# Kernel optimization log

Measured on AMD Instinct MI355X. Metric: run time of the kernel, lower is better.

## Reference

```python
import jax, jax.numpy as jnp
from jax import lax
import numpy as np

K = 4          # kernel_size
DEPTH = 2      # sig_depth
B, S, CIN = 64, 1024, 5
H1, H2 = 64, 16
OUT = 32
C1 = H2 + CIN + 1            # channels entering signature1 (include_original + include_time)
SIG_C1 = C1 + C1 * C1        # 506
SIG_C2 = H2 + H2 * H2        # 272


def setup_inputs() -> dict:
    key = jax.random.key(0)
    ks = jax.random.split(key, 12)
    def w(k, shape, fan_in):
        return jax.random.normal(k, shape, jnp.float32) * (1.0 / np.sqrt(fan_in))
    inp = {}
    inp["x"] = jax.random.normal(ks[0], (B, S, CIN), jnp.float32)
    inp["lengths"] = jax.random.randint(ks[1], (B,), S // 2, S + 1)
    # Augment 1: Conv1d(CIN->H1, k=K), Conv1d(H1->H1, 1), Conv1d(H1->H2, 1)
    inp["a1_w0"] = w(ks[2], (H1, CIN, K), CIN * K); inp["a1_b0"] = jnp.zeros((H1,), jnp.float32)
    inp["a1_w1"] = w(ks[3], (H1, H1, 1), H1);       inp["a1_b1"] = jnp.zeros((H1,), jnp.float32)
    inp["a1_w2"] = w(ks[4], (H2, H1, 1), H1);       inp["a1_b2"] = jnp.zeros((H2,), jnp.float32)
    # Augment 2: Conv1d(SIG_C1->H1, k=K), Conv1d(H1->H1, 1), Conv1d(H1->H2, 1)
    inp["a2_w0"] = w(ks[5], (H1, SIG_C1, K), SIG_C1 * K); inp["a2_b0"] = jnp.zeros((H1,), jnp.float32)
    inp["a2_w1"] = w(ks[6], (H1, H1, 1), H1);             inp["a2_b1"] = jnp.zeros((H1,), jnp.float32)
    inp["a2_w2"] = w(ks[7], (H2, H1, 1), H1);             inp["a2_b2"] = jnp.zeros((H2,), jnp.float32)
    inp["lin_w"] = w(ks[8], (OUT, SIG_C2), SIG_C2)
    inp["lin_b"] = jnp.zeros((OUT,), jnp.float32)
    return inp


def _conv1d(x, w, b):
    # x: (B, C, L), w: (O, I, k) -> (B, O, L-k+1), VALID (no padding), stride 1
    y = lax.conv_general_dilated(x, w, (1,), 'VALID', dimension_numbers=('NCH', 'OIH', 'NCH'))
    return y + b[None, :, None]


def _augment(x, ws, bs, kernel_size, include_original, include_time):
    # signatory.Augment: relu between convs, none after last; concat [original_trunc, time, conv_out]
    b_, s_, _ = x.shape
    L = s_ - kernel_size + 1
    pieces = []
    if include_original:
        pieces.append(x[:, kernel_size - 1:, :])
    if include_time:
        t = jnp.linspace(0.0, 1.0, L, dtype=x.dtype)
        pieces.append(jnp.broadcast_to(t[None, :, None], (b_, L, 1)))
    h = jnp.swapaxes(x, 1, 2)
    h = _conv1d(h, ws[0], bs[0])
    for wi, bi in zip(ws[1:], bs[1:]):
        h = _conv1d(jax.nn.relu(h), wi, bi)
    pieces.append(jnp.swapaxes(h, 1, 2))
    return jnp.concatenate(pieces, axis=2)


def _sig_exp(dx, depth):
    # tensor-algebra exp of a linear segment: level k = dx^{\otimes k} / k!
    levels = [dx]
    cur = dx
    for k in range(2, depth + 1):
        cur = (cur[..., :, None] * dx[..., None, :]).reshape(dx.shape[:-1] + (-1,)) / k
        levels.append(cur)
    return levels


def _chen(a, b, depth):
    # Chen's relation: (a*b)_k = a_k + sum_{i=1}^{k-1} a_i (x) b_{k-i} + b_k
    out = []
    for k in range(1, depth + 1):
        acc = a[k - 1] + b[k - 1]
        for i in range(1, k):
            acc = acc + (a[i - 1][:, :, None] * b[k - i - 1][:, None, :]).reshape(acc.shape)
        out.append(acc)
    return tuple(out)


def _signature(x, depth, stream):
    # basepoint=True: prepend zero point, so increments are diff with zero prepended
    b_, s_, c_ = x.shape
    dx = jnp.diff(x, axis=1, prepend=jnp.zeros((b_, 1, c_), x.dtype))
    exps = tuple(jnp.moveaxis(e, 1, 0) for e in _sig_exp(dx, depth))  # each (S, B, c^k)
    init = tuple(jnp.zeros((b_, c_ ** k), x.dtype) for k in range(1, depth + 1))  # identity (levels=0)
    def step(carry, e):
        new = _chen(carry, e, depth)
        return new, (new if stream else None)
    carry, ys = lax.scan(step, init, exps)
    if stream:
        return jnp.concatenate([jnp.moveaxis(y, 0, 1) for y in ys], axis=2)
    return jnp.concatenate(carry, axis=1)


def _become_constant(x, lengths):
    # y[i,j] = x[i,j] if j < lengths[i] else x[i, lengths[i]-1]
    b_, s_, _ = x.shape
    idx = jnp.minimum(jnp.arange(s_)[None, :], (lengths - 1)[:, None])
    return x[jnp.arange(b_)[:, None], idx]


def reference(x, lengths, a1_w0, a1_b0, a1_w1, a1_b1, a1_w2, a1_b2,
              a2_w0, a2_b0, a2_w1, a2_b1, a2_w2, a2_b2, lin_w, lin_b):
    h = _augment(x, (a1_w0, a1_w1, a1_w2), (a1_b0, a1_b1, a1_b2), K, True, True)   # (B, S-K+1, C1)
    s1 = _signature(h, DEPTH, True)                                                # (B, S-K+1, SIG_C1)
    h2 = _augment(s1, (a2_w0, a2_w1, a2_w2), (a2_b0, a2_b1, a2_b2), K, False, False)  # (B, S-2K+2, H2)
    adj = lengths - 2 * K + 2
    h2 = _become_constant(h2, adj)
    s2 = _signature(h2, DEPTH, False)                                              # (B, SIG_C2)
    return s2 @ lin_w.T + lin_b
```

## Files before the change

kernel.cpp:

```cpp
#include <hip/hip_runtime.h>
#include <hip/hip_bf16.h>

#define B_    64
#define S_    1024
#define CIN   5
#define K_    4
#define H1    64
#define H2    16
#define OUT_  32
#define L1_   1021
#define C1    22
#define C1SQ  484
#define SIGC1 506
#define L2_   1018
#define SIGC2 272
#define NCH   32
#define CH1   32
#define RPAD  1032
#define CPAD  512

typedef __attribute__((ext_vector_type(8))) short short8;
typedef __attribute__((ext_vector_type(16))) float f32x16;

__device__ __forceinline__ unsigned short f2bf(float v) {
  __hip_bfloat16 h = __float2bfloat16(v);
  return *reinterpret_cast<unsigned short*>(&h);
}
__device__ __forceinline__ float bf2f(unsigned short u) {
  __hip_bfloat16 h;
  *reinterpret_cast<unsigned short*>(&h) = u;
  return __bfloat162float(h);
}

__global__ __launch_bounds__(256) void aug1_kernel(
    const float* __restrict__ x,
    const float* __restrict__ w0, const float* __restrict__ b0,
    const float* __restrict__ w1, const float* __restrict__ b1,
    const float* __restrict__ w2, const float* __restrict__ b2,
    float* __restrict__ h) {
  int b = blockIdx.y;
  int l = blockIdx.x * 256 + threadIdx.x;
  if (l >= L1_) return;
  const float* xb = x + (size_t)b * S_ * CIN;

  float t1[H1];
#pragma unroll
  for (int o = 0; o < H1; ++o) t1[o] = b0[o];
  for (int j = 0; j < K_; ++j) {
    for (int c = 0; c < CIN; ++c) {
      float xv = xb[(l + j) * CIN + c];
#pragma unroll
      for (int o = 0; o < H1; ++o) t1[o] += xv * w0[o * (CIN * K_) + c * K_ + j];
    }
  }
#pragma unroll
  for (int o = 0; o < H1; ++o) t1[o] = fmaxf(t1[o], 0.f);

  float t3[H2];
#pragma unroll
  for (int q = 0; q < H2; ++q) t3[q] = b2[q];
  for (int ch = 0; ch < 4; ++ch) {
    float t2c[16];
    for (int oc = 0; oc < 16; ++oc) {
      int o = ch * 16 + oc;
      float a = b1[o];
#pragma unroll
      for (int i = 0; i < H1; ++i) a += t1[i] * w1[o * H1 + i];
      t2c[oc] = fmaxf(a, 0.f);
    }
#pragma unroll
    for (int q = 0; q < H2; ++q) {
      float a = t3[q];
#pragma unroll
      for (int oc = 0; oc < 16; ++oc) a += t2c[oc] * w2[q * H1 + ch * 16 + oc];
      t3[q] = a;
    }
  }

  float* hr = h + ((size_t)b * L1_ + l) * C1;
#pragma unroll
  for (int c = 0; c < CIN; ++c) hr[c] = xb[(l + K_ - 1) * CIN + c];
  hr[CIN] = (float)l / (float)(L1_ - 1);
#pragma unroll
  for (int q = 0; q < H2; ++q) hr[CIN + 1 + q] = t3[q];
}

__global__ __launch_bounds__(512) void sig1a_kernel(const float* __restrict__ h, float* __restrict__ s2tot) {
  int k = blockIdx.x, b = blockIdx.y;
  int tid = threadIdx.x;
  if (tid >= C1SQ) return;
  int start = k * CH1, end = min(start + CH1 - 1, L1_ - 1);
  const float* hb = h + (size_t)b * L1_ * C1;
  int i = tid / C1, j = tid - i * C1;
  float hpi = 0.f, hpj = 0.f;
  if (k > 0) {
    hpi = hb[(start - 1) * C1 + i];
    hpj = hb[(start - 1) * C1 + j];
  }
  float pi = 0.f, pj = 0.f, s2 = 0.f;
  for (int t = start; t <= end; ++t) {
    float ci = hb[t * C1 + i] - hpi;
    float cj = hb[t * C1 + j] - hpj;
    float dj = cj - pj;
    s2 += pi * dj + 0.5f * (ci - pi) * dj;
    pi = ci;
    pj = cj;
  }
  s2tot[((size_t)b * NCH + k) * C1SQ + tid] = s2;
}

__global__ __launch_bounds__(512) void sig1b_kernel(const float* __restrict__ h, const float* __restrict__ s2tot,
                                                    float* __restrict__ s2pre) {
  int b = blockIdx.x;
  int tid = threadIdx.x;
  const float* hb = h + (size_t)b * L1_ * C1;
  __shared__ float bv[NCH + 1][C1];
  for (int idx = tid; idx < (NCH + 1) * C1; idx += 512) {
    int kk = idx / C1, c = idx - kk * C1;
    float v = 0.f;
    if (kk > 0) v = hb[min(CH1 * kk - 1, L1_ - 1) * C1 + c];
    bv[kk][c] = v;
  }
  int i = tid / C1, j = tid - i * C1;
  __syncthreads();
  if (tid >= C1SQ) return;
  float s2p = 0.f;
  for (int k = 0; k < NCH; ++k) {
    size_t idx = ((size_t)b * NCH + k) * C1SQ + tid;
    s2pre[idx] = s2p;
    s2p += bv[k][i] * (bv[k + 1][j] - bv[k][j]) + s2tot[idx];
  }
}

__global__ __launch_bounds__(512) void sig1c_kernel(const float* __restrict__ h, const float* __restrict__ s2pre,
                                                    unsigned short* __restrict__ s1hi,
                                                    unsigned short* __restrict__ s1lo) {
  int k = blockIdx.x, b = blockIdx.y;
  int tid = threadIdx.x;
  int start = k * CH1, end = min(start + CH1 - 1, L1_ - 1);
  const float* hb = h + (size_t)b * L1_ * C1;
  unsigned short* hio = s1hi + (size_t)b * RPAD * CPAD;
  unsigned short* loo = s1lo + (size_t)b * RPAD * CPAD;
  int c = (tid < C1SQ) ? (C1 + tid) : ((tid < C1SQ + C1) ? (tid - C1SQ) : tid);
  int cbase = (c >> 6) * 64 + (c & 7);
  int cg = (c >> 3) & 7;

  if (tid < C1SQ) {
    int i = tid / C1, j = tid - i * C1;
    float hpi = 0.f, hpj = 0.f;
    if (k > 0) {
      hpi = hb[(start - 1) * C1 + i];
      hpj = hb[(start - 1) * C1 + j];
    }
    float s2p = s2pre[((size_t)b * NCH + k) * C1SQ + tid];
    float pi = 0.f, pj = 0.f, s2 = 0.f;
    for (int t = start; t <= end; ++t) {
      float ci = hb[t * C1 + i] - hpi;
      float cj = hb[t * C1 + j] - hpj;
      float dj = cj - pj;
      s2 += pi * dj + 0.5f * (ci - pi) * dj;
      pi = ci;
      pj = cj;
      float v = s2p + hpi * cj + s2;
      unsigned short hb16 = f2bf(v);
      unsigned short lb16 = f2bf(v - bf2f(hb16));
      size_t off = (size_t)t * CPAD + cbase + ((size_t)(cg ^ (t & 7)) << 3);
      hio[off] = hb16;
      loo[off] = lb16;
    }
  } else if (tid < C1SQ + C1) {
    int cc = tid - C1SQ;
    for (int t = start; t <= end; ++t) {
      float v = hb[t * C1 + cc];
      unsigned short hb16 = f2bf(v);
      unsigned short lb16 = f2bf(v - bf2f(hb16));
      size_t off = (size_t)t * CPAD + cbase + ((size_t)(cg ^ (t & 7)) << 3);
      hio[off] = hb16;
      loo[off] = lb16;
    }
  } else {
    for (int t = start; t <= end; ++t) {
      size_t off = (size_t)t * CPAD + cbase + ((size_t)(cg ^ (t & 7)) << 3);
      hio[off] = 0;
      loo[off] = 0;
    }
  }
}

__global__ __launch_bounds__(256) void wt2_kernel(const float* __restrict__ w0,
                                                  unsigned short* __restrict__ bhi,
                                                  unsigned short* __restrict__ blo) {
  int idx = blockIdx.x * 256 + threadIdx.x;
  if (idx >= 2 * 128 * 64 * 8) return;
  int e = idx & 7;
  int lane = (idx >> 3) & 63;
  int ksg = (idx >> 9) & 127;
  int ot = idx >> 16;
  int j = ksg >> 5, cc = (ksg >> 2) & 7, ks = ksg & 3;
  int o = ot * 32 + (lane & 31);
  int c = cc * 64 + ks * 16 + (lane >> 5) * 8 + e;
  float v = (c < SIGC1) ? w0[o * (SIGC1 * K_) + c * K_ + j] : 0.f;
  unsigned short hb16 = f2bf(v);
  bhi[idx] = hb16;
  blo[idx] = f2bf(v - bf2f(hb16));
}

__global__ __launch_bounds__(512) void conv2pw_kernel(
    const unsigned short* __restrict__ s1hi, const unsigned short* __restrict__ s1lo,
    const unsigned short* __restrict__ bpkhi, const unsigned short* __restrict__ bpklo,
    const float* __restrict__ b0,
    const float* __restrict__ w1, const float* __restrict__ b1,
    const float* __restrict__ w2, const float* __restrict__ b2,
    float* __restrict__ h2) {
  __shared__ __align__(16) char smem[153600];
  int tid = threadIdx.x;
  int lane = tid & 63, w = tid >> 6;
  int wm = w >> 1, wo = w & 1;
  int b = blockIdx.y, l0 = blockIdx.x * 256;
  const char* ghi = (const char*)(s1hi + (size_t)b * RPAD * CPAD) + (size_t)l0 * 1024;
  const char* glo = (const char*)(s1lo + (size_t)b * RPAD * CPAD) + (size_t)l0 * 1024;
  const char* bhg = (const char*)bpkhi;
  const char* blg = (const char*)bpklo;
  char* Ah = smem;
  char* Al = smem + 33792;
  char* Bs = smem + 67584;
  f32x16 a0HH = {}, a0HL = {}, a0LH = {}, a1HH = {}, a1HL = {}, a1LH = {};
  int khalf = lane >> 5;
  int r0 = 64 * wm + (lane & 31);

  for (int cc = 0; cc < 8; ++cc) {
    if (cc) __syncthreads();
    {
      int srcoff = cc * 128 + (lane & 7) * 16;
      for (int li = w; li < 33; li += 8) {
        int rowoff = (li * 8 + (lane >> 3)) * 1024;
        __builtin_amdgcn_global_load_lds(
            (const __attribute__((address_space(1))) void*)(ghi + rowoff + srcoff),
            (__attribute__((address_space(3))) void*)(Ah + li * 1024), 16, 0, 0);
        __builtin_amdgcn_global_load_lds(
            (const __attribute__((address_space(1))) void*)(glo + rowoff + srcoff),
            (__attribute__((address_space(3))) void*)(Al + li * 1024), 16, 0, 0);
      }
    }
    for (int s = w; s < 64; s += 8) {
      int p = s >> 2, ot = (s >> 1) & 1, plane = s & 1;
      int jj = p >> 2, ks = p & 3;
      int ksg = jj * 32 + cc * 4 + ks;
      const char* src = (plane ? blg : bhg) + (size_t)(ot * 128 + ksg) * 1024 + lane * 16;
      __builtin_amdgcn_global_load_lds(
          (const __attribute__((address_space(1))) void*)src,
          (__attribute__((address_space(3))) void*)(Bs + ((p * 2 + ot) * 2 + plane) * 1024), 16, 0, 0);
    }
    __syncthreads();
#pragma unroll
    for (int j = 0; j < 4; ++j) {
      int ra0 = r0 + j, ra1 = ra0 + 32;
      int rx0 = ra0 & 7, rx1 = ra1 & 7;
      const char* a0b = Ah + ra0 * 128;
      const char* a0bl = Al + ra0 * 128;
      const char* a1b = Ah + ra1 * 128;
      const char* a1bl = Al + ra1 * 128;
#pragma unroll
      for (int ks = 0; ks < 4; ++ks) {
        int p = j * 4 + ks;
        const char* bb = Bs + (size_t)((p * 2 + wo) * 2) * 1024 + lane * 16;
        short8 b_h = *(const short8*)bb;
        short8 b_l = *(const short8*)(bb + 1024);
        int g0 = ((ks * 2 + khalf) ^ rx0) << 4;
        int g1 = ((ks * 2 + khalf) ^ rx1) << 4;
        short8 v0h = *(const short8*)(a0b + g0);
        short8 v0l = *(const short8*)(a0bl + g0);
        short8 v1h = *(const short8*)(a1b + g1);
        short8 v1l = *(const short8*)(a1bl + g1);
        a0HH = __builtin_amdgcn_mfma_f32_32x32x16_bf16(v0h, b_h, a0HH, 0, 0, 0);
        a0HL = __builtin_amdgcn_mfma_f32_32x32x16_bf16(v0h, b_l, a0HL, 0, 0, 0);
        a0LH = __builtin_amdgcn_mfma_f32_32x32x16_bf16(v0l, b_h, a0LH, 0, 0, 0);
        a1HH = __builtin_amdgcn_mfma_f32_32x32x16_bf16(v1h, b_h, a1HH, 0, 0, 0);
        a1HL = __builtin_amdgcn_mfma_f32_32x32x16_bf16(v1h, b_l, a1HL, 0, 0, 0);
        a1LH = __builtin_amdgcn_mfma_f32_32x32x16_bf16(v1l, b_h, a1LH, 0, 0, 0);
      }
    }
  }
  __syncthreads();
  float* t1s = (float*)smem;
  float* t2s = (float*)(smem + 66560);
  float* wl = (float*)(smem + 133120);
  for (int i2 = tid; i2 < 4096; i2 += 512) wl[i2] = w1[i2];
  for (int i2 = tid; i2 < 1024; i2 += 512) wl[4096 + i2] = w2[i2];
  {
    int col = 32 * wo + (lane & 31);
    float bbv = b0[col];
    int rbase = 64 * wm + 4 * (lane >> 5);
#pragma unroll
    for (int rg = 0; rg < 16; ++rg) {
      int row = (rg & 3) + 8 * (rg >> 2) + rbase;
      t1s[row * 65 + col] = fmaxf(a0HH[rg] + a0HL[rg] + a0LH[rg] + bbv, 0.f);
      t1s[(row + 32) * 65 + col] = fmaxf(a1HH[rg] + a1HL[rg] + a1LH[rg] + bbv, 0.f);
    }
  }
  __syncthreads();
  {
    int row = tid & 255, qh = tid >> 8;
    float tr[64];
#pragma unroll
    for (int i2 = 0; i2 < 64; ++i2) tr[i2] = t1s[row * 65 + i2];
#pragma unroll
    for (int oc = 0; oc < 32; ++oc) {
      int o = qh * 32 + oc;
      float a = b1[o];
      const float4* wr = (const float4*)(wl + o * 64);
#pragma unroll
      for (int i4 = 0; i4 < 16; ++i4) {
        float4 wv = wr[i4];
        a += tr[i4 * 4] * wv.x + tr[i4 * 4 + 1] * wv.y +
             tr[i4 * 4 + 2] * wv.z + tr[i4 * 4 + 3] * wv.w;
      }
      t2s[row * 65 + o] = fmaxf(a, 0.f);
    }
  }
  __syncthreads();
  {
    int row = tid & 255, ph = tid >> 8;
    int l = l0 + row;
    if (l < L2_) {
      float tr2[64];
#pragma unroll
      for (int i2 = 0; i2 < 64; ++i2) tr2[i2] = t2s[row * 65 + i2];
      float* outr = h2 + ((size_t)b * L2_ + l) * H2;
#pragma unroll
      for (int pp = 0; pp < 8; ++pp) {
        int pch = ph * 8 + pp;
        float a = b2[pch];
        const float4* wr = (const float4*)(wl + 4096 + pch * 64);
#pragma unroll
        for (int i4 = 0; i4 < 16; ++i4) {
          float4 wv = wr[i4];
          a += tr2[i4 * 4] * wv.x + tr2[i4 * 4 + 1] * wv.y +
               tr2[i4 * 4 + 2] * wv.z + tr2[i4 * 4 + 3] * wv.w;
        }
        outr[pch] = a;
      }
    }
  }
}

__global__ __launch_bounds__(256) void sig2a_kernel(const float* __restrict__ h2, const int* __restrict__ lengths,
                                                    float* __restrict__ s2tot2) {
  int k = blockIdx.x, b = blockIdx.y;
  int tid = threadIdx.x;
  int i = tid >> 4, j = tid & 15;
  int adjm1 = lengths[b] - (2 * K_ - 2) - 1;
  int start = k * CH1, end = min(start + CH1 - 1, L2_ - 1);
  size_t oidx = ((size_t)b * NCH + k) * 256 + tid;
  if (k > 0 && start - 1 >= adjm1) {
    s2tot2[oidx] = 0.f;
    return;
  }
  const float* h2b = h2 + (size_t)b * L2_ * H2;
  float hpi = 0.f, hpj = 0.f;
  if (k > 0) {
    int row = min(start - 1, adjm1);
    hpi = h2b[row * H2 + i];
    hpj = h2b[row * H2 + j];
  }
  float pi = 0.f, pj = 0.f, s2 = 0.f;
  for (int t = start; t <= end; ++t) {
    int row = min(t, adjm1);
    float ci = h2b[row * H2 + i] - hpi;
    float cj = h2b[row * H2 + j] - hpj;
    float dj = cj - pj;
    s2 += pi * dj + 0.5f * (ci - pi) * dj;
    pi = ci;
    pj = cj;
  }
  s2tot2[oidx] = s2;
}

__global__ __launch_bounds__(256) void sig2b_kernel(const float* __restrict__ h2, const int* __restrict__ lengths,
                                                    const float* __restrict__ s2tot2,
                                                    const float* __restrict__ lin_w, const float* __restrict__ lin_b,
                                                    float* __restrict__ out) {
  int b = blockIdx.x;
  int tid = threadIdx.x;
  int i = tid >> 4, j = tid & 15;
  int adjm1 = lengths[b] - (2 * K_ - 2) - 1;
  const float* h2b = h2 + (size_t)b * L2_ * H2;
  __shared__ float bv[NCH + 1][H2];
  __shared__ float s2s[SIGC2];
  for (int idx = tid; idx < (NCH + 1) * H2; idx += 256) {
    int kk = idx >> 4, c = idx & 15;
    float v = 0.f;
    if (kk > 0) {
      int row = min(min(CH1 * kk - 1, L2_ - 1), adjm1);
      v = h2b[row * H2 + c];
    }
    bv[kk][c] = v;
  }
  __syncthreads();
  float s2 = 0.f;
  for (int k = 0; k < NCH; ++k) {
    s2 += bv[k][i] * (bv[k + 1][j] - bv[k][j]) + s2tot2[((size_t)b * NCH + k) * 256 + tid];
  }
  s2s[H2 + tid] = s2;
  if (tid < H2) s2s[tid] = bv[NCH][tid];
  __syncthreads();
  if (tid < OUT_) {
    float a = lin_b[tid];
    for (int c = 0; c < SIGC2; ++c) a += s2s[c] * lin_w[tid * SIGC2 + c];
    out[b * OUT_ + tid] = a;
  }
}

extern "C" void kernel_launch(void* const* d_in, const int* in_sizes, int n_in,
                              void* d_out, int out_size, void* d_ws, size_t ws_size,
                              hipStream_t stream) {
  const float* x      = (const float*)d_in[0];
  const int*   lengths= (const int*)d_in[1];
  const float* a1_w0  = (const float*)d_in[2];
  const float* a1_b0  = (const float*)d_in[3];
  const float* a1_w1  = (const float*)d_in[4];
  const float* a1_b1  = (const float*)d_in[5];
  const float* a1_w2  = (const float*)d_in[6];
  const float* a1_b2  = (const float*)d_in[7];
  const float* a2_w0  = (const float*)d_in[8];
  const float* a2_b0  = (const float*)d_in[9];
  const float* a2_w1  = (const float*)d_in[10];
  const float* a2_b1  = (const float*)d_in[11];
  const float* a2_w2  = (const float*)d_in[12];
  const float* a2_b2  = (const float*)d_in[13];
  const float* lin_w  = (const float*)d_in[14];
  const float* lin_b  = (const float*)d_in[15];
  float* outp = (float*)d_out;

  float* ws = (float*)d_ws;
  float* h = ws;
  unsigned short* s1hi = (unsigned short*)(ws + 1437568);
  unsigned short* s1lo = s1hi + (size_t)B_ * RPAD * CPAD;
  unsigned short* bpkhi = (unsigned short*)(ws + 35254144);
  unsigned short* bpklo = bpkhi + 131072;
  float* h2 = ws + 35385216;
  float* s2tot1 = ws + 36427648;
  float* s2pre1 = ws + 37418880;
  float* s2tot2 = (float*)s1hi;

  aug1_kernel<<<dim3(4, B_), 256, 0, stream>>>(x, a1_w0, a1_b0, a1_w1, a1_b1, a1_w2, a1_b2, h);
  wt2_kernel<<<(2 * 128 * 64 * 8 + 255) / 256, 256, 0, stream>>>(a2_w0, bpkhi, bpklo);
  sig1a_kernel<<<dim3(NCH, B_), 512, 0, stream>>>(h, s2tot1);
  sig1b_kernel<<<B_, 512, 0, stream>>>(h, s2tot1, s2pre1);
  sig1c_kernel<<<dim3(NCH, B_), 512, 0, stream>>>(h, s2pre1, s1hi, s1lo);
  conv2pw_kernel<<<dim3(4, B_), 512, 0, stream>>>(s1hi, s1lo, bpkhi, bpklo, a2_b0,
                                                  a2_w1, a2_b1, a2_w2, a2_b2, h2);
  sig2a_kernel<<<dim3(NCH, B_), 256, 0, stream>>>(h2, lengths, s2tot2);
  sig2b_kernel<<<B_, 256, 0, stream>>>(h2, lengths, s2tot2, lin_w, lin_b, outp);
}
```

Baseline: 298.9 us.

## Fuse signature-1 stream computation into conv2 GEMM, dropping the global bf16 staging

The per-timestep level-2 signature stream is now computed directly inside the conv2 kernel and written as split bf16 hi/lo into LDS, so the large global s1hi/s1lo buffers (about 64x1032x512x2x2 bytes) are no longer written and re-read. The chunk prefix pass is reduced to a 3-tile sig1a plus an in-block serial prefix over earlier tiles, which removes the sig1b and sig1c launches. In exchange, the GEMM kernel does extra ALU work per channel chunk, needs more LDS, and adds an intra-block two-pass scan with an extra barrier per chunk. Occupancy and latency hiding in the GEMM may also suffer.

```diff
diff --git a/kernel.cpp b/kernel.cpp
--- a/kernel.cpp
+++ b/kernel.cpp
@@ -16,8 +16,6 @@
 #define SIGC2 272
 #define NCH   32
 #define CH1   32
-#define RPAD  1032
-#define CPAD  512
 
 typedef __attribute__((ext_vector_type(8))) short short8;
 typedef __attribute__((ext_vector_type(16))) float f32x16;
@@ -85,20 +83,20 @@
   for (int q = 0; q < H2; ++q) hr[CIN + 1 + q] = t3[q];
 }
 
-__global__ __launch_bounds__(512) void sig1a_kernel(const float* __restrict__ h, float* __restrict__ s2tot) {
-  int k = blockIdx.x, b = blockIdx.y;
+__global__ __launch_bounds__(512) void sig1a_kernel(const float* __restrict__ h, float* __restrict__ tot1) {
+  int kt = blockIdx.x, b = blockIdx.y;
   int tid = threadIdx.x;
   if (tid >= C1SQ) return;
-  int start = k * CH1, end = min(start + CH1 - 1, L1_ - 1);
+  int start = kt * 256;
   const float* hb = h + (size_t)b * L1_ * C1;
   int i = tid / C1, j = tid - i * C1;
   float hpi = 0.f, hpj = 0.f;
-  if (k > 0) {
+  if (kt > 0) {
     hpi = hb[(start - 1) * C1 + i];
     hpj = hb[(start - 1) * C1 + j];
   }
   float pi = 0.f, pj = 0.f, s2 = 0.f;
-  for (int t = start; t <= end; ++t) {
+  for (int t = start; t < start + 256; ++t) {
     float ci = hb[t * C1 + i] - hpi;
     float cj = hb[t * C1 + j] - hpj;
     float dj = cj - pj;
@@ -106,85 +104,7 @@
     pi = ci;
     pj = cj;
   }
-  s2tot[((size_t)b * NCH + k) * C1SQ + tid] = s2;
-}
-
-__global__ __launch_bounds__(512) void sig1b_kernel(const float* __restrict__ h, const float* __restrict__ s2tot,
-                                                    float* __restrict__ s2pre) {
-  int b = blockIdx.x;
-  int tid = threadIdx.x;
-  const float* hb = h + (size_t)b * L1_ * C1;
-  __shared__ float bv[NCH + 1][C1];
-  for (int idx = tid; idx < (NCH + 1) * C1; idx += 512) {
-    int kk = idx / C1, c = idx - kk * C1;
-    float v = 0.f;
-    if (kk > 0) v = hb[min(CH1 * kk - 1, L1_ - 1) * C1 + c];
-    bv[kk][c] = v;
-  }
-  int i = tid / C1, j = tid - i * C1;
-  __syncthreads();
-  if (tid >= C1SQ) return;
-  float s2p = 0.f;
-  for (int k = 0; k < NCH; ++k) {
-    size_t idx = ((size_t)b * NCH + k) * C1SQ + tid;
-    s2pre[idx] = s2p;
-    s2p += bv[k][i] * (bv[k + 1][j] - bv[k][j]) + s2tot[idx];
-  }
-}
-
-__global__ __launch_bounds__(512) void sig1c_kernel(const float* __restrict__ h, const float* __restrict__ s2pre,
-                                                    unsigned short* __restrict__ s1hi,
-                                                    unsigned short* __restrict__ s1lo) {
-  int k = blockIdx.x, b = blockIdx.y;
-  int tid = threadIdx.x;
-  int start = k * CH1, end = min(start + CH1 - 1, L1_ - 1);
-  const float* hb = h + (size_t)b * L1_ * C1;
-  unsigned short* hio = s1hi + (size_t)b * RPAD * CPAD;
-  unsigned short* loo = s1lo + (size_t)b * RPAD * CPAD;
-  int c = (tid < C1SQ) ? (C1 + tid) : ((tid < C1SQ + C1) ? (tid - C1SQ) : tid);
-  int cbase = (c >> 6) * 64 + (c & 7);
-  int cg = (c >> 3) & 7;
-
-  if (tid < C1SQ) {
-    int i = tid / C1, j = tid - i * C1;
-    float hpi = 0.f, hpj = 0.f;
-    if (k > 0) {
-      hpi = hb[(start - 1) * C1 + i];
-      hpj = hb[(start - 1) * C1 + j];
-    }
-    float s2p = s2pre[((size_t)b * NCH + k) * C1SQ + tid];
-    float pi = 0.f, pj = 0.f, s2 = 0.f;
-    for (int t = start; t <= end; ++t) {
-      float ci = hb[t * C1 + i] - hpi;
-      float cj = hb[t * C1 + j] - hpj;
-      float dj = cj - pj;
-      s2 += pi * dj + 0.5f * (ci - pi) * dj;
-      pi = ci;
-      pj = cj;
-      float v = s2p + hpi * cj + s2;
-      unsigned short hb16 = f2bf(v);
-      unsigned short lb16 = f2bf(v - bf2f(hb16));
-      size_t off = (size_t)t * CPAD + cbase + ((size_t)(cg ^ (t & 7)) << 3);
-      hio[off] = hb16;
-      loo[off] = lb16;
-    }
-  } else if (tid < C1SQ + C1) {
-    int cc = tid - C1SQ;
-    for (int t = start; t <= end; ++t) {
-      float v = hb[t * C1 + cc];
-      unsigned short hb16 = f2bf(v);
-      unsigned short lb16 = f2bf(v - bf2f(hb16));
-      size_t off = (size_t)t * CPAD + cbase + ((size_t)(cg ^ (t & 7)) << 3);
-      hio[off] = hb16;
-      loo[off] = lb16;
-    }
-  } else {
-    for (int t = start; t <= end; ++t) {
-      size_t off = (size_t)t * CPAD + cbase + ((size_t)(cg ^ (t & 7)) << 3);
-      hio[off] = 0;
-      loo[off] = 0;
-    }
-  }
+  tot1[((size_t)b * 4 + kt) * C1SQ + tid] = s2;
 }
 
 __global__ __launch_bounds__(256) void wt2_kernel(const float* __restrict__ w0,
@@ -206,42 +126,59 @@
 }
 
 __global__ __launch_bounds__(512) void conv2pw_kernel(
-    const unsigned short* __restrict__ s1hi, const unsigned short* __restrict__ s1lo,
+    const float* __restrict__ h, const float* __restrict__ tot1,
     const unsigned short* __restrict__ bpkhi, const unsigned short* __restrict__ bpklo,
     const float* __restrict__ b0,
     const float* __restrict__ w1, const float* __restrict__ b1,
     const float* __restrict__ w2, const float* __restrict__ b2,
     float* __restrict__ h2) {
-  __shared__ __align__(16) char smem[153600];
+  __shared__ __align__(16) char smem[160768];
   int tid = threadIdx.x;
   int lane = tid & 63, w = tid >> 6;
   int wm = w >> 1, wo = w & 1;
-  int b = blockIdx.y, l0 = blockIdx.x * 256;
-  const char* ghi = (const char*)(s1hi + (size_t)b * RPAD * CPAD) + (size_t)l0 * 1024;
-  const char* glo = (const char*)(s1lo + (size_t)b * RPAD * CPAD) + (size_t)l0 * 1024;
+  int k = blockIdx.x, b = blockIdx.y, l0 = k * 256;
+  const float* hb = h + (size_t)b * L1_ * C1;
   const char* bhg = (const char*)bpkhi;
   const char* blg = (const char*)bpklo;
-  char* Ah = smem;
-  char* Al = smem + 33792;
-  char* Bs = smem + 67584;
+  float* hs = (float*)smem;
+  char* Ah = smem + 23552;
+  char* Al = smem + 57344;
+  char* Bs = smem + 91136;
+  float* gsum = (float*)(smem + 156672);
+  float* s2pl = (float*)(smem + 158720);
+
+  for (int idx = tid; idx < 265 * C1; idx += 512) {
+    int r = idx / C1, c = idx - r * C1;
+    float v = 0.f;
+    if (!(k == 0 && r == 0)) {
+      int hr = l0 - 1 + r;
+      if (hr > L1_ - 1) hr = L1_ - 1;
+      v = hb[hr * C1 + c];
+    }
+    hs[idx] = v;
+  }
+  if (tid < C1SQ) {
+    int i = tid / C1, j = tid - i * C1;
+    float s2pv = 0.f;
+    for (int kp = 0; kp < k; ++kp) {
+      float bvi = 0.f, bvj = 0.f;
+      if (kp > 0) {
+        bvi = hb[(256 * kp - 1) * C1 + i];
+        bvj = hb[(256 * kp - 1) * C1 + j];
+      }
+      float bv1j = hb[(256 * (kp + 1) - 1) * C1 + j];
+      s2pv += bvi * (bv1j - bvj) + tot1[((size_t)b * 4 + kp) * C1SQ + tid];
+    }
+    s2pl[tid] = s2pv;
+  }
+  __syncthreads();
+
   f32x16 a0HH = {}, a0HL = {}, a0LH = {}, a1HH = {}, a1HL = {}, a1LH = {};
   int khalf = lane >> 5;
   int r0 = 64 * wm + (lane & 31);
 
   for (int cc = 0; cc < 8; ++cc) {
     if (cc) __syncthreads();
-    {
-      int srcoff = cc * 128 + (lane & 7) * 16;
-      for (int li = w; li < 33; li += 8) {
-        int rowoff = (li * 8 + (lane >> 3)) * 1024;
-        __builtin_amdgcn_global_load_lds(
-            (const __attribute__((address_space(1))) void*)(ghi + rowoff + srcoff),
-            (__attribute__((address_space(3))) void*)(Ah + li * 1024), 16, 0, 0);
-        __builtin_amdgcn_global_load_lds(
-            (const __attribute__((address_space(1))) void*)(glo + rowoff + srcoff),
-            (__attribute__((address_space(3))) void*)(Al + li * 1024), 16, 0, 0);
-      }
-    }
     for (int s = w; s < 64; s += 8) {
       int p = s >> 2, ot = (s >> 1) & 1, plane = s & 1;
       int jj = p >> 2, ks = p & 3;
@@ -250,6 +187,62 @@
       __builtin_amdgcn_global_load_lds(
           (const __attribute__((address_space(1))) void*)src,
           (__attribute__((address_space(3))) void*)(Bs + ((p * 2 + ot) * 2 + plane) * 1024), 16, 0, 0);
+    }
+    int c = cc * 64 + lane;
+    bool isS2 = (c >= C1 && c < SIGC1);
+    int ii = 0, jj2 = 0;
+    if (isS2) {
+      int idx = c - C1;
+      ii = idx / C1;
+      jj2 = idx - ii * C1;
+    }
+    float hpi = hs[ii], hpj = hs[jj2];
+    int u0 = w * 33;
+    {
+      float pi = hs[u0 * C1 + ii] - hpi;
+      float pj = hs[u0 * C1 + jj2] - hpj;
+      float loc = 0.f;
+#pragma unroll 3
+      for (int s = 0; s < 33; ++s) {
+        int u = u0 + s;
+        float ci = hs[(u + 1) * C1 + ii] - hpi;
+        float cj = hs[(u + 1) * C1 + jj2] - hpj;
+        float dj = cj - pj;
+        loc += pi * dj + 0.5f * (ci - pi) * dj;
+        pi = ci;
+        pj = cj;
+      }
+      gsum[w * 64 + lane] = loc;
+    }
+    __syncthreads();
+    {
+      float s2r = isS2 ? s2pl[c - C1] : 0.f;
+      for (int gp = 0; gp < w; ++gp) s2r += gsum[gp * 64 + lane];
+      float pi = hs[u0 * C1 + ii] - hpi;
+      float pj = hs[u0 * C1 + jj2] - hpj;
+#pragma unroll 3
+      for (int s = 0; s < 33; ++s) {
+        int u = u0 + s;
+        float v;
+        if (isS2) {
+          float ci = hs[(u + 1) * C1 + ii] - hpi;
+          float cj = hs[(u + 1) * C1 + jj2] - hpj;
+          float dj = cj - pj;
+          s2r += pi * dj + 0.5f * (ci - pi) * dj;
+          pi = ci;
+          pj = cj;
+          v = s2r + hpi * cj;
+        } else if (c < C1) {
+          v = hs[(u + 1) * C1 + c];
+        } else {
+          v = 0.f;
+        }
+        unsigned short hb16 = f2bf(v);
+        unsigned short lb16 = f2bf(v - bf2f(hb16));
+        int boff = u * 128 + ((((lane >> 3) ^ (u & 7))) << 4) + (lane & 7) * 2;
+        *(unsigned short*)(Ah + boff) = hb16;
+        *(unsigned short*)(Al + boff) = lb16;
+      }
     }
     __syncthreads();
 #pragma unroll
@@ -434,21 +427,16 @@
 
   float* ws = (float*)d_ws;
   float* h = ws;
-  unsigned short* s1hi = (unsigned short*)(ws + 1437568);
-  unsigned short* s1lo = s1hi + (size_t)B_ * RPAD * CPAD;
-  unsigned short* bpkhi = (unsigned short*)(ws + 35254144);
+  unsigned short* bpkhi = (unsigned short*)(ws + 1437568);
   unsigned short* bpklo = bpkhi + 131072;
-  float* h2 = ws + 35385216;
-  float* s2tot1 = ws + 36427648;
-  float* s2pre1 = ws + 37418880;
-  float* s2tot2 = (float*)s1hi;
+  float* h2 = ws + 1568640;
+  float* tot1 = ws + 2611072;
+  float* s2tot2 = ws + 2734976;
 
   aug1_kernel<<<dim3(4, B_), 256, 0, stream>>>(x, a1_w0, a1_b0, a1_w1, a1_b1, a1_w2, a1_b2, h);
   wt2_kernel<<<(2 * 128 * 64 * 8 + 255) / 256, 256, 0, stream>>>(a2_w0, bpkhi, bpklo);
-  sig1a_kernel<<<dim3(NCH, B_), 512, 0, stream>>>(h, s2tot1);
-  sig1b_kernel<<<B_, 512, 0, stream>>>(h, s2tot1, s2pre1);
-  sig1c_kernel<<<dim3(NCH, B_), 512, 0, stream>>>(h, s2pre1, s1hi, s1lo);
-  conv2pw_kernel<<<dim3(4, B_), 512, 0, stream>>>(s1hi, s1lo, bpkhi, bpklo, a2_b0,
+  sig1a_kernel<<<dim3(3, B_), 512, 0, stream>>>(h, tot1);
+  conv2pw_kernel<<<dim3(4, B_), 512, 0, stream>>>(h, tot1, bpkhi, bpklo, a2_b0,
                                                   a2_w1, a2_b1, a2_w2, a2_b2, h2);
   sig2a_kernel<<<dim3(NCH, B_), 256, 0, stream>>>(h2, lengths, s2tot2);
   sig2b_kernel<<<B_, 256, 0, stream>>>(h2, lengths, s2tot2, lin_w, lin_b, outp);
```

Result: faster. 265.0 us (-11.3%).
